# Optimization experiments

Hardware: AMD Instinct MI355X
Metric: run time of the kernel (lower is better)

The kernel has to match this reference:

```python
import jax, jax.numpy as jnp
import numpy as np

NUM_HEADS = 8
TOPK_RATIO = 0.1


def setup_inputs() -> dict:
    key = jax.random.key(0)
    ks = jax.random.split(key, 5)
    B, N, C = 1, 8192, 512
    S = 16              # num_frames
    K = 4               # clusters
    x = jax.random.normal(ks[0], (B, N, C), dtype=jnp.float32)
    w_qkv = jax.random.normal(ks[1], (3 * C, C), dtype=jnp.float32) * (C ** -0.5)
    b_qkv = jax.random.normal(ks[2], (3 * C,), dtype=jnp.float32) * 0.02
    w_proj = jax.random.normal(ks[3], (C, C), dtype=jnp.float32) * (C ** -0.5)
    b_proj = jax.random.normal(ks[4], (C,), dtype=jnp.float32) * 0.02
    keyframes = jnp.arange(K, dtype=jnp.int64 if jax.config.jax_enable_x64 else jnp.int32) * (S // K)  # [0,4,8,12]
    clusters = jnp.arange(S, dtype=keyframes.dtype).reshape(K, S // K)  # 4 clusters of 4 frames
    return {"x": x, "w_qkv": w_qkv, "b_qkv": b_qkv, "w_proj": w_proj,
            "b_proj": b_proj, "keyframes": keyframes, "clusters": clusters,
            "num_frames": S}


def _hierarchy_attn(q, k, v, keyframes, clusters, num_frames):
    # q,k,v: [B,H,N,D]
    B, H, N, D = q.shape
    scale = D ** -0.5
    tpf = N // num_frames                     # tokens per frame
    K = clusters.shape[0]
    tok = jnp.arange(tpf)
    # keyframe query token indices: [K*tpf]
    key_q_idx = (keyframes[:, None] * tpf + tok[None, :]).reshape(-1)
    q_proto = q[:, :, key_q_idx, :]           # [B,H,K*tpf,D]
    # proto attention scores vs all keys: [B,H,K*tpf,N]
    scores = jnp.einsum('bhqd,bhnd->bhqn', q_proto * scale, k)
    # aggregate per cluster (over batch, heads, keyframe tokens) -> [K,N]
    agg = scores.reshape(B, H, K, tpf, N).mean(axis=(0, 1, 3))
    topk_num = max(1, int(tpf * K * TOPK_RATIO))
    _, topk_idx = jax.lax.top_k(agg, topk_num)          # [K, T]
    # cluster query token indices: [K, M] with M = frames_per_cluster*tpf
    cluster_q_idx = (clusters[:, :, None] * tpf + tok[None, None, :]).reshape(K, -1)
    q_c = q[:, :, cluster_q_idx, :]           # [B,H,K,M,D]
    k_c = k[:, :, topk_idx, :]                # [B,H,K,T,D]
    v_c = v[:, :, topk_idx, :]                # [B,H,K,T,D]
    attn = jax.nn.softmax(jnp.einsum('bhkmd,bhktd->bhkmt', q_c * scale, k_c), axis=-1)
    x_c = jnp.einsum('bhkmt,bhktd->bhkmd', attn, v_c)   # [B,H,K,M,D]
    x_out = jnp.zeros_like(q)
    x_out = x_out.at[:, :, cluster_q_idx.reshape(-1), :].set(
        x_c.reshape(B, H, K * x_c.shape[3], D))
    return x_out


def reference(x, w_qkv, b_qkv, w_proj, b_proj, keyframes, clusters, num_frames):
    B, N, C = x.shape
    H = NUM_HEADS
    D = C // H
    qkv = (x @ w_qkv.T + b_qkv).reshape(B, N, 3, H, D)
    qkv = jnp.transpose(qkv, (2, 0, 3, 1, 4))           # [3,B,H,N,D]
    q, k, v = qkv[0], qkv[1], qkv[2]
    x_out = _hierarchy_attn(q, k, v, keyframes, clusters, num_frames)  # [B,H,N,D]
    x_out = jnp.transpose(x_out, (0, 2, 1, 3)).reshape(B, N, C)
    return x_out @ w_proj.T + b_proj
```

## Files before the change

### kernel.cpp

```cpp
#include <hip/hip_runtime.h>
#include <hip/hip_bf16.h>

#define N_TOK 8192
#define C_DIM 512
#define NH 8
#define DH 64
#define KCLUST 4
#define TPF 512
#define TOPK 204
#define KVPAD 256
#define MPC 2048

#define WS_WQH    0
#define WS_WPH    393216
#define WS_QHI    524288
#define WS_KC     2621440
#define WS_VC     2883584
#define WS_XAHI   3145728
#define WS_XBARP  5242880
#define WS_QBAR   5275648
#define WS_G      5277696
#define WS_AGG    5279744
#define WS_TOPK   5312512

using frag16 = __attribute__((ext_vector_type(8))) short;
using f32x4  = __attribute__((ext_vector_type(4))) float;

__device__ __forceinline__ unsigned short f2bf(float x) {
  unsigned u = __float_as_uint(x);
  return (unsigned short)((u + 0x7fffu + ((u >> 16) & 1u)) >> 16);
}
__device__ __forceinline__ float bf2f(unsigned short h) {
  return __uint_as_float(((unsigned)h) << 16);
}
__device__ __forceinline__ unsigned pkbf(float a, float b) {
  __hip_bfloat162 t = __float22bfloat162_rn(make_float2(a, b));
  return *reinterpret_cast<unsigned*>(&t);
}

__global__ __launch_bounds__(256) void prep(
    const float* __restrict__ w_qkv, const float* __restrict__ w_proj,
    const float* __restrict__ x, const int* __restrict__ keyframes,
    unsigned short* __restrict__ wqh, unsigned short* __restrict__ wph,
    float* __restrict__ xbarp) {
  const int bx = blockIdx.x, tid = threadIdx.x;
  if (bx < 1024) {
    const float* src = (bx < 768) ? w_qkv : w_proj;
    unsigned short* dst = (bx < 768) ? wqh : wph;
    int i = ((bx < 768) ? bx : (bx - 768)) * 256 + tid;
    float4 v = reinterpret_cast<const float4*>(src)[i];
    reinterpret_cast<uint2*>(dst)[i] = make_uint2(pkbf(v.x, v.y), pkbf(v.z, v.w));
  } else {
    int b = bx - 1024, kk = b >> 4, s = b & 15;
    int base = keyframes[kk] * TPF + s * 32;
    float a0 = 0.f, a1 = 0.f;
    for (int t = 0; t < 32; t++) {
      a0 += x[(size_t)(base + t) * C_DIM + tid];
      a1 += x[(size_t)(base + t) * C_DIM + tid + 256];
    }
    xbarp[(kk * 16 + s) * C_DIM + tid] = a0;
    xbarp[(kk * 16 + s) * C_DIM + tid + 256] = a1;
  }
}

#define APAN 1032
#define BUFS 8256
__global__ __launch_bounds__(256) void gemm_qkv2(
    const float* __restrict__ x, const unsigned short* __restrict__ Bhi,
    const float* __restrict__ bias, const int* __restrict__ topk,
    unsigned short* __restrict__ qhi, unsigned short* __restrict__ kc,
    unsigned short* __restrict__ vc) {
  __shared__ short pool[17408];
  const int tid = threadIdx.x;
  const int bid = blockIdx.x;
  const bool is_kv = bid >= 256;
  int j0, m0 = 0, kk = 0, mloc = 0;
  if (!is_kv) {
    const int grp = bid >> 5;
    const int rem = bid & 31;
    j0 = (rem >> 3) * 128;
    m0 = (grp * 8 + (rem & 7)) * 128;
  } else {
    const int b2 = bid - 256;
    kk = b2 >> 4;
    const int sub = b2 & 15;
    mloc = (sub >> 3) * 128;
    j0 = 512 + (sub & 7) * 128;
  }
  const int wave = tid >> 6, lane = tid & 63;
  const int wr = wave >> 1, wc = wave & 1;
  const int qd = lane >> 4, ln = lane & 15;

  const int r0 = tid >> 2, p0 = tid & 3;
  const int r1 = r0 + 64;
  const float4 *pA0, *pA1;
  if (!is_kv) {
    pA0 = reinterpret_cast<const float4*>(x + (size_t)(m0 + r0) * C_DIM) + p0 * 2;
    pA1 = reinterpret_cast<const float4*>(x + (size_t)(m0 + r1) * C_DIM) + p0 * 2;
  } else {
    int t0i = mloc + r0, t1i = mloc + r1;
    if (t0i > TOPK - 1) t0i = TOPK - 1;
    if (t1i > TOPK - 1) t1i = TOPK - 1;
    const int tok0 = topk[kk * TOPK + t0i];
    const int tok1 = topk[kk * TOPK + t1i];
    pA0 = reinterpret_cast<const float4*>(x + (size_t)tok0 * C_DIM) + p0 * 2;
    pA1 = reinterpret_cast<const float4*>(x + (size_t)tok1 * C_DIM) + p0 * 2;
  }
  const unsigned short* pB0 = Bhi + (size_t)(j0 + r0) * C_DIM + p0 * 8;
  const unsigned short* pB1 = Bhi + (size_t)(j0 + r1) * C_DIM + p0 * 8;

  f32x4 acc[4][4] = {};

  float4 fa[4];
  uint4 rb[2];
  fa[0] = pA0[0]; fa[1] = pA0[1];
  fa[2] = pA1[0]; fa[3] = pA1[1];
  rb[0] = *reinterpret_cast<const uint4*>(pB0);
  rb[1] = *reinterpret_cast<const uint4*>(pB1);

  {
    *reinterpret_cast<uint4*>(&pool[p0 * APAN + r0 * 8]) =
        make_uint4(pkbf(fa[0].x, fa[0].y), pkbf(fa[0].z, fa[0].w),
                   pkbf(fa[1].x, fa[1].y), pkbf(fa[1].z, fa[1].w));
    *reinterpret_cast<uint4*>(&pool[p0 * APAN + r1 * 8]) =
        make_uint4(pkbf(fa[2].x, fa[2].y), pkbf(fa[2].z, fa[2].w),
                   pkbf(fa[3].x, fa[3].y), pkbf(fa[3].z, fa[3].w));
    *reinterpret_cast<uint4*>(&pool[4 * APAN + p0 * APAN + r0 * 8]) = rb[0];
    *reinterpret_cast<uint4*>(&pool[4 * APAN + p0 * APAN + r1 * 8]) = rb[1];
  }
  __syncthreads();

  int cur = 0;
#pragma unroll
  for (int it = 0; it < 16; it++) {
    if (it < 15) {
      int k4 = (it + 1) * 8;
      fa[0] = pA0[k4]; fa[1] = pA0[k4 + 1];
      fa[2] = pA1[k4]; fa[3] = pA1[k4 + 1];
      rb[0] = *reinterpret_cast<const uint4*>(pB0 + (it + 1) * 32);
      rb[1] = *reinterpret_cast<const uint4*>(pB1 + (it + 1) * 32);
    }
    const int bb = cur * BUFS;
    frag16 a_h[4], b_h[4];
#pragma unroll
    for (int i = 0; i < 4; i++) {
      int row = wr * 64 + i * 16 + ln;
      a_h[i] = *reinterpret_cast<const frag16*>(&pool[bb + qd * APAN + row * 8]);
    }
#pragma unroll
    for (int j = 0; j < 4; j++) {
      int row = wc * 64 + j * 16 + ln;
      b_h[j] = *reinterpret_cast<const frag16*>(&pool[bb + 4 * APAN + qd * APAN + row * 8]);
    }
#pragma unroll
    for (int i = 0; i < 4; i++)
#pragma unroll
      for (int j = 0; j < 4; j++)
        acc[i][j] = __builtin_amdgcn_mfma_f32_16x16x32_bf16(a_h[i], b_h[j], acc[i][j], 0, 0, 0);

    if (it < 15) {
      const int nb = (cur ^ 1) * BUFS;
      *reinterpret_cast<uint4*>(&pool[nb + p0 * APAN + r0 * 8]) =
          make_uint4(pkbf(fa[0].x, fa[0].y), pkbf(fa[0].z, fa[0].w),
                     pkbf(fa[1].x, fa[1].y), pkbf(fa[1].z, fa[1].w));
      *reinterpret_cast<uint4*>(&pool[nb + p0 * APAN + r1 * 8]) =
          make_uint4(pkbf(fa[2].x, fa[2].y), pkbf(fa[2].z, fa[2].w),
                     pkbf(fa[3].x, fa[3].y), pkbf(fa[3].z, fa[3].w));
      *reinterpret_cast<uint4*>(&pool[nb + 4 * APAN + p0 * APAN + r0 * 8]) = rb[0];
      *reinterpret_cast<uint4*>(&pool[nb + 4 * APAN + p0 * APAN + r1 * 8]) = rb[1];
    }
    __syncthreads();
    cur ^= 1;
  }

  const int sel = j0 >> 9;
  const float qscale = (sel == 0) ? 0.125f : 1.0f;
  short* sh = pool;

#pragma unroll
  for (int i = 0; i < 4; i++)
#pragma unroll
    for (int j = 0; j < 4; j++) {
      int jcol = wc * 64 + j * 16 + ln;
      float bv = bias[j0 + jcol];
#pragma unroll
      for (int r = 0; r < 4; r++) {
        int mrow = wr * 64 + i * 16 + qd * 4 + r;
        sh[mrow * 136 + jcol] = (short)f2bf((acc[i][j][r] + bv) * qscale);
      }
    }
  __syncthreads();
  if (!is_kv) {
#pragma unroll
    for (int p = 0; p < 8; p++) {
      int u = tid + p * 256;
      int row = u >> 4, c = (u & 15) * 8;
      int hh = ((j0 + c) >> 6) & 7, d0 = c & 63;
      *reinterpret_cast<uint4*>(qhi + ((size_t)hh * N_TOK + m0 + row) * DH + d0) =
          *reinterpret_cast<const uint4*>(&sh[row * 136 + c]);
    }
  } else {
    unsigned short* dstc = (sel == 1) ? kc : vc;
#pragma unroll
    for (int p = 0; p < 8; p++) {
      int u = tid + p * 256;
      int row = u >> 4, c = (u & 15) * 8;
      int hh = ((j0 + c) >> 6) & 7, d0 = c & 63;
      *reinterpret_cast<uint4*>(
          dstc + (((size_t)kk * 8 + hh) * KVPAD + mloc + row) * DH + d0) =
          *reinterpret_cast<const uint4*>(&sh[row * 136 + c]);
    }
  }
}

__global__ __launch_bounds__(256) void qbar_k(const float* __restrict__ w_qkv,
                                              const float* __restrict__ b_qkv,
                                              const float* __restrict__ xbarp,
                                              float* __restrict__ qbar) {
  __shared__ float xs[C_DIM];
  __shared__ float red[256];
  int blk = blockIdx.x, h = blk >> 2, kk = blk & 3, tid = threadIdx.x;
  for (int i = tid; i < C_DIM; i += 256) {
    float a = 0.f;
    for (int s = 0; s < 16; s++) a += xbarp[(kk * 16 + s) * C_DIM + i];
    xs[i] = a * (1.f / 512.f);
  }
  __syncthreads();
  int d = tid & 63, pp = tid >> 6;
  const float* wrow = w_qkv + (size_t)(h * 64 + d) * C_DIM + pp * 128;
  float a = 0.f;
  for (int c = 0; c < 128; c++) a += wrow[c] * xs[pp * 128 + c];
  red[tid] = a;
  __syncthreads();
  if (pp == 0)
    qbar[(h * 4 + kk) * 64 + d] = red[d] + red[64 + d] + red[128 + d] + red[192 + d] +
                                  b_qkv[h * 64 + d];
}

__global__ __launch_bounds__(256) void g_full(const float* __restrict__ w_qkv,
                                              const float* __restrict__ qbar,
                                              float* __restrict__ g) {
  __shared__ float qs[C_DIM];
  __shared__ float red[256];
  int kk = blockIdx.x >> 3, cs = blockIdx.x & 7, tid = threadIdx.x;
  for (int i = tid; i < C_DIM; i += 256)
    qs[i] = qbar[((i >> 6) * 4 + kk) * 64 + (i & 63)];
  __syncthreads();
  int jg = tid >> 6, c = tid & 63;
  float a = 0.f;
  const float* wk = w_qkv + (size_t)C_DIM * C_DIM + cs * 64 + c;
  for (int j = jg * 128; j < jg * 128 + 128; j++)
    a += qs[j] * wk[(size_t)j * C_DIM];
  red[tid] = a;
  __syncthreads();
  if (jg == 0)
    g[kk * C_DIM + cs * 64 + c] = red[c] + red[64 + c] + red[128 + c] + red[192 + c];
}

__global__ __launch_bounds__(256) void agg2_kernel(const float* __restrict__ x,
                                                   const float* __restrict__ g,
                                                   float* __restrict__ agg) {
  __shared__ float gs[KCLUST][C_DIM];
  int tid = threadIdx.x;
  for (int i = tid; i < KCLUST * C_DIM; i += 256) gs[i >> 9][i & 511] = g[i];
  __syncthreads();
  int wave = tid >> 6, lane = tid & 63;
  int n = blockIdx.x * 4 + wave;
  const float4* xp = reinterpret_cast<const float4*>(x + (size_t)n * C_DIM);
  float4 xa = xp[lane], xb = xp[lane + 64];
  float a[4];
#pragma unroll
  for (int kk = 0; kk < 4; kk++) {
    const float4* gpv = reinterpret_cast<const float4*>(&gs[kk][0]);
    float4 ga = gpv[lane], gb2 = gpv[lane + 64];
    a[kk] = xa.x * ga.x + xa.y * ga.y + xa.z * ga.z + xa.w * ga.w +
            xb.x * gb2.x + xb.y * gb2.y + xb.z * gb2.z + xb.w * gb2.w;
  }
#pragma unroll
  for (int off = 32; off >= 1; off >>= 1) {
    a[0] += __shfl_xor(a[0], off);
    a[1] += __shfl_xor(a[1], off);
    a[2] += __shfl_xor(a[2], off);
    a[3] += __shfl_xor(a[3], off);
  }
  if (lane == 0) {
    agg[0 * N_TOK + n] = a[0];
    agg[1 * N_TOK + n] = a[1];
    agg[2 * N_TOK + n] = a[2];
    agg[3 * N_TOK + n] = a[3];
  }
}

__device__ __forceinline__ int block_scan_incl(int v, int* wsum, int tid) {
  int lane = tid & 63, wv = tid >> 6;
#pragma unroll
  for (int off = 1; off < 64; off <<= 1) {
    int t = __shfl_up(v, off, 64);
    if (lane >= off) v += t;
  }
  if (lane == 63) wsum[wv] = v;
  __syncthreads();
  if (wv > 0) v += wsum[0];
  if (wv > 1) v += wsum[1];
  if (wv > 2) v += wsum[2];
  __syncthreads();
  return v;
}

__global__ __launch_bounds__(256) void topk_kernel(const float* __restrict__ agg,
                                                   int* __restrict__ topk) {
  __shared__ unsigned sk[N_TOK];
  __shared__ int hist[256];
  __shared__ int scn[256];
  __shared__ int wsum[4];
  __shared__ int sel_bin, sel_rem;
  int kk = blockIdx.x, tid = threadIdx.x;
  const float* row = agg + (size_t)kk * N_TOK;

  for (int i = tid; i < N_TOK; i += 256) {
    unsigned u = __float_as_uint(row[i]);
    sk[i] = (u & 0x80000000u) ? ~u : (u | 0x80000000u);
  }
  __syncthreads();

  unsigned prefix = 0;
  int remaining = TOPK;
#pragma unroll
  for (int rnd = 3; rnd >= 0; rnd--) {
    int shift = rnd * 8;
    hist[tid] = 0;
    __syncthreads();
    for (int i = tid; i < N_TOK; i += 256) {
      unsigned key = sk[i];
      bool in = (rnd == 3) || ((key >> (shift + 8)) == prefix);
      if (in) atomicAdd(&hist[(key >> shift) & 255], 1);
    }
    __syncthreads();
    int sv = block_scan_incl(hist[255 - tid], wsum, tid);
    scn[tid] = sv;
    __syncthreads();
    int b = tid;
    int cgt = (b == 255) ? 0 : scn[254 - b];
    if (cgt < remaining && remaining <= cgt + hist[b]) {
      sel_bin = b;
      sel_rem = remaining - cgt;
    }
    __syncthreads();
    prefix = (prefix << 8) | (unsigned)sel_bin;
    remaining = sel_rem;
    __syncthreads();
  }
  unsigned kth = prefix;

  int* out_row = topk + kk * TOPK;
  int base = tid * 32;

  int cA = 0;
  for (int i = 0; i < 32; i++) cA += (sk[base + i] > kth) ? 1 : 0;
  int sA = block_scan_incl(cA, wsum, tid);
  scn[tid] = sA;
  __syncthreads();
  int exclA = sA - cA;
  int G = scn[255];
  int p = exclA;
  for (int i = 0; i < 32; i++)
    if (sk[base + i] > kth) out_row[p++] = base + i;
  __syncthreads();

  int cB = 0;
  for (int i = 0; i < 32; i++) cB += (sk[base + i] == kth) ? 1 : 0;
  int sB = block_scan_incl(cB, wsum, tid);
  int exclB = sB - cB;
  int pos = G + exclB;
  for (int i = 0; i < 32; i++) {
    if (sk[base + i] == kth) {
      if (pos < TOPK) out_row[pos] = base + i;
      pos++;
    }
  }
}

__global__ __launch_bounds__(256) void flash_mfma(
    const unsigned short* __restrict__ qhi, const unsigned short* __restrict__ kc,
    const unsigned short* __restrict__ vc, const int* __restrict__ clusters,
    unsigned short* __restrict__ xahi) {
  __shared__ short Ks[64 * 72];
  __shared__ short Vs[64 * 72];
  __shared__ short Ps[128 * 72];
  const int tid = threadIdx.x;
  const int qb = blockIdx.x, kk = blockIdx.y, h = blockIdx.z;
  const int wave = tid >> 6, lane = tid & 63;
  const int ln = lane & 15, qd = lane >> 4;

  const int q_local0 = qb * 128;
  const int frame = clusters[kk * 4 + (q_local0 >> 9)];
  const int tokbase = frame * TPF + (q_local0 & 511);
  const size_t kvbase = ((size_t)kk * 8 + h) * KVPAD * DH;

  frag16 qa_h[2][2];
#pragma unroll
  for (int mt = 0; mt < 2; mt++) {
    const int tok_m = tokbase + wave * 32 + mt * 16 + ln;
    const unsigned short* qr_h = qhi + ((size_t)h * N_TOK + tok_m) * DH;
#pragma unroll
    for (int s = 0; s < 2; s++)
      qa_h[mt][s] = *reinterpret_cast<const frag16*>(qr_h + s * 32 + qd * 8);
  }

  f32x4 acc_o[2][4] = {};
  float lsum[2][4] = {};

  for (int t0 = 0; t0 < 192; t0 += 64) {
#pragma unroll
    for (int i = 0; i < 2; i++) {
      int u = tid + i * 256;
      int r = u >> 3, oct = u & 7;
      *reinterpret_cast<frag16*>(&Ks[r * 72 + oct * 8]) =
          *reinterpret_cast<const frag16*>(kc + kvbase + (size_t)(t0 + r) * DH + oct * 8);
    }
    {
      int tk = (tid & 15) * 4, td = (tid >> 4) * 4;
      uint2 w2[4];
#pragma unroll
      for (int i = 0; i < 4; i++)
        w2[i] = *reinterpret_cast<const uint2*>(vc + kvbase + (size_t)(t0 + tk + i) * DH + td);
#pragma unroll
      for (int dd = 0; dd < 4; dd++) {
        unsigned s0 = (dd < 2) ? (w2[0].x >> (16 * dd)) : (w2[0].y >> (16 * (dd - 2)));
        unsigned s1 = (dd < 2) ? (w2[1].x >> (16 * dd)) : (w2[1].y >> (16 * (dd - 2)));
        unsigned s2 = (dd < 2) ? (w2[2].x >> (16 * dd)) : (w2[2].y >> (16 * (dd - 2)));
        unsigned s3 = (dd < 2) ? (w2[3].x >> (16 * dd)) : (w2[3].y >> (16 * (dd - 2)));
        *reinterpret_cast<uint2*>(&Vs[(td + dd) * 72 + tk]) =
            make_uint2((s0 & 0xffffu) | (s1 << 16), (s2 & 0xffffu) | (s3 << 16));
      }
    }
    __syncthreads();

#pragma unroll
    for (int mt = 0; mt < 2; mt++) {
      f32x4 sacc[4] = {};
#pragma unroll
      for (int c = 0; c < 4; c++) {
#pragma unroll
        for (int s = 0; s < 2; s++) {
          frag16 bh = *reinterpret_cast<const frag16*>(&Ks[(c * 16 + ln) * 72 + s * 32 + qd * 8]);
          sacc[c] = __builtin_amdgcn_mfma_f32_16x16x32_bf16(qa_h[mt][s], bh, sacc[c], 0, 0, 0);
        }
      }
#pragma unroll
      for (int c = 0; c < 4; c++) {
#pragma unroll
        for (int r = 0; r < 4; r++) {
          float p = __expf(sacc[c][r]);
          lsum[mt][r] += p;
          Ps[(wave * 32 + mt * 16 + qd * 4 + r) * 72 + c * 16 + ln] = (short)f2bf(p);
        }
      }
    }

#pragma unroll
    for (int mt = 0; mt < 2; mt++)
#pragma unroll
      for (int s = 0; s < 2; s++) {
        frag16 pa = *reinterpret_cast<const frag16*>(
            &Ps[(wave * 32 + mt * 16 + ln) * 72 + s * 32 + qd * 8]);
#pragma unroll
        for (int dt = 0; dt < 4; dt++) {
          frag16 vb = *reinterpret_cast<const frag16*>(&Vs[(dt * 16 + ln) * 72 + s * 32 + qd * 8]);
          acc_o[mt][dt] = __builtin_amdgcn_mfma_f32_16x16x32_bf16(pa, vb, acc_o[mt][dt], 0, 0, 0);
        }
      }
    __syncthreads();
  }

  {
    const int t0 = 192;
#pragma unroll
    for (int i = 0; i < 2; i++) {
      int u = tid + i * 256;
      int r = u >> 3, oct = u & 7;
      *reinterpret_cast<frag16*>(&Ks[r * 72 + oct * 8]) =
          *reinterpret_cast<const frag16*>(kc + kvbase + (size_t)(t0 + r) * DH + oct * 8);
    }
    {
      int tk = (tid & 15) * 4, td = (tid >> 4) * 4;
      uint2 w2[4];
#pragma unroll
      for (int i = 0; i < 4; i++)
        w2[i] = *reinterpret_cast<const uint2*>(vc + kvbase + (size_t)(t0 + tk + i) * DH + td);
#pragma unroll
      for (int dd = 0; dd < 4; dd++) {
        unsigned s0 = (dd < 2) ? (w2[0].x >> (16 * dd)) : (w2[0].y >> (16 * (dd - 2)));
        unsigned s1 = (dd < 2) ? (w2[1].x >> (16 * dd)) : (w2[1].y >> (16 * (dd - 2)));
        unsigned s2 = (dd < 2) ? (w2[2].x >> (16 * dd)) : (w2[2].y >> (16 * (dd - 2)));
        unsigned s3 = (dd < 2) ? (w2[3].x >> (16 * dd)) : (w2[3].y >> (16 * (dd - 2)));
        *reinterpret_cast<uint2*>(&Vs[(td + dd) * 72 + tk]) =
            make_uint2((s0 & 0xffffu) | (s1 << 16), (s2 & 0xffffu) | (s3 << 16));
      }
    }
    __syncthreads();

#pragma unroll
    for (int mt = 0; mt < 2; mt++) {
      f32x4 sacc = {};
#pragma unroll
      for (int s = 0; s < 2; s++) {
        frag16 bh = *reinterpret_cast<const frag16*>(&Ks[ln * 72 + s * 32 + qd * 8]);
        sacc = __builtin_amdgcn_mfma_f32_16x16x32_bf16(qa_h[mt][s], bh, sacc, 0, 0, 0);
      }
#pragma unroll
      for (int r = 0; r < 4; r++) {
        float p = (ln < 12) ? __expf(sacc[r]) : 0.f;
        lsum[mt][r] += p;
        int prow = (wave * 32 + mt * 16 + qd * 4 + r) * 72;
        Ps[prow + ln] = (short)f2bf(p);
        Ps[prow + 16 + ln] = 0;
      }
    }

#pragma unroll
    for (int mt = 0; mt < 2; mt++) {
      frag16 pa = *reinterpret_cast<const frag16*>(
          &Ps[(wave * 32 + mt * 16 + ln) * 72 + qd * 8]);
#pragma unroll
      for (int dt = 0; dt < 4; dt++) {
        frag16 vb = *reinterpret_cast<const frag16*>(&Vs[(dt * 16 + ln) * 72 + qd * 8]);
        acc_o[mt][dt] = __builtin_amdgcn_mfma_f32_16x16x32_bf16(pa, vb, acc_o[mt][dt], 0, 0, 0);
      }
    }
  }

#pragma unroll
  for (int mt = 0; mt < 2; mt++)
#pragma unroll
    for (int r = 0; r < 4; r++) {
      float l = lsum[mt][r];
      l += __shfl_xor(l, 1);
      l += __shfl_xor(l, 2);
      l += __shfl_xor(l, 4);
      l += __shfl_xor(l, 8);
      lsum[mt][r] = 1.f / l;
    }

#pragma unroll
  for (int mt = 0; mt < 2; mt++)
#pragma unroll
    for (int dt = 0; dt < 4; dt++)
#pragma unroll
      for (int r = 0; r < 4; r++)
        Ps[(wave * 32 + mt * 16 + qd * 4 + r) * 72 + dt * 16 + ln] =
            (short)f2bf(acc_o[mt][dt][r] * lsum[mt][r]);
  __syncthreads();
#pragma unroll
  for (int p = 0; p < 4; p++) {
    int u = tid + p * 256;
    int row = u >> 3, c = (u & 7) * 8;
    *reinterpret_cast<uint4*>(xahi + (size_t)(tokbase + row) * C_DIM + h * DH + c) =
        *reinterpret_cast<const uint4*>(&Ps[row * 72 + c]);
  }
}

__global__ __launch_bounds__(256) void gemm_proj(
    const unsigned short* __restrict__ Ahi, const unsigned short* __restrict__ Bhi,
    const float* __restrict__ bias, float* __restrict__ out) {
  __shared__ short pool[12288];
  short* As = pool;
  short* Bs = pool + 4096;
  const int tid = threadIdx.x;
  const int bid = blockIdx.x;
  const int grp = bid / 32;
  const int rem = bid - grp * 32;
  const int jblk = rem >> 3;
  const int m_idx = grp * 8 + (rem & 7);
  const int j0 = jblk * 128;
  const int m0 = m_idx * 64;
  const int wave = tid >> 6, lane = tid & 63;
  const int rh = wave >> 1, ch = wave & 1;
  const int qd = lane >> 4, ln = lane & 15;

  const int arow = tid & 63, ap = tid >> 6;
  const int brow = tid & 127, bp = tid >> 7;
  const unsigned short* pA = Ahi + (size_t)(m0 + arow) * C_DIM + ap * 8;
  const unsigned short* pB0 = Bhi + (size_t)(j0 + brow) * C_DIM + bp * 8;
  const unsigned short* pB1 = pB0 + 16;

  f32x4 acc[2][4] = {};

  uint4 ra = *reinterpret_cast<const uint4*>(pA);
  uint4 rb0 = *reinterpret_cast<const uint4*>(pB0);
  uint4 rb1 = *reinterpret_cast<const uint4*>(pB1);
  *reinterpret_cast<uint4*>(&As[ap * 512 + arow * 8]) = ra;
  *reinterpret_cast<uint4*>(&Bs[bp * 1024 + brow * 8]) = rb0;
  *reinterpret_cast<uint4*>(&Bs[(bp + 2) * 1024 + brow * 8]) = rb1;
  __syncthreads();

  int cur = 0;
#pragma unroll
  for (int it = 0; it < 16; it++) {
    if (it < 15) {
      int k = (it + 1) * 32;
      ra = *reinterpret_cast<const uint4*>(pA + k);
      rb0 = *reinterpret_cast<const uint4*>(pB0 + k);
      rb1 = *reinterpret_cast<const uint4*>(pB1 + k);
    }
    frag16 a_h[2], b_h[4];
#pragma unroll
    for (int i = 0; i < 2; i++)
      a_h[i] = *reinterpret_cast<const frag16*>(&As[cur * 2048 + qd * 512 + (rh * 32 + i * 16 + ln) * 8]);
#pragma unroll
    for (int j = 0; j < 4; j++)
      b_h[j] = *reinterpret_cast<const frag16*>(&Bs[cur * 4096 + qd * 1024 + (ch * 64 + j * 16 + ln) * 8]);
#pragma unroll
    for (int i = 0; i < 2; i++)
#pragma unroll
      for (int j = 0; j < 4; j++)
        acc[i][j] = __builtin_amdgcn_mfma_f32_16x16x32_bf16(a_h[i], b_h[j], acc[i][j], 0, 0, 0);
    if (it < 15) {
      int nxt = cur ^ 1;
      *reinterpret_cast<uint4*>(&As[nxt * 2048 + ap * 512 + arow * 8]) = ra;
      *reinterpret_cast<uint4*>(&Bs[nxt * 4096 + bp * 1024 + brow * 8]) = rb0;
      *reinterpret_cast<uint4*>(&Bs[nxt * 4096 + (bp + 2) * 1024 + brow * 8]) = rb1;
      __syncthreads();
      cur = nxt;
    }
  }

  float* sh32 = reinterpret_cast<float*>(pool);
#pragma unroll
  for (int chp = 0; chp < 2; chp++) {
    __syncthreads();
    if (ch == chp) {
#pragma unroll
      for (int i = 0; i < 2; i++)
#pragma unroll
        for (int j = 0; j < 4; j++) {
          int jcol = j * 16 + ln;
          float bv = bias[j0 + chp * 64 + jcol];
#pragma unroll
          for (int r = 0; r < 4; r++)
            sh32[(rh * 32 + i * 16 + qd * 4 + r) * 68 + jcol] = acc[i][j][r] + bv;
        }
    }
    __syncthreads();
#pragma unroll
    for (int p = 0; p < 4; p++) {
      int u = tid + p * 256;
      int row = u >> 4, c4 = (u & 15) * 4;
      *reinterpret_cast<float4*>(out + (size_t)(m0 + row) * C_DIM + j0 + chp * 64 + c4) =
          *reinterpret_cast<const float4*>(&sh32[row * 68 + c4]);
    }
  }
}

extern "C" void kernel_launch(void* const* d_in, const int* in_sizes, int n_in,
                              void* d_out, int out_size, void* d_ws, size_t ws_size,
                              hipStream_t stream) {
  const float* x = (const float*)d_in[0];
  const float* w_qkv = (const float*)d_in[1];
  const float* b_qkv = (const float*)d_in[2];
  const float* w_proj = (const float*)d_in[3];
  const float* b_proj = (const float*)d_in[4];
  const int* keyframes = (const int*)d_in[5];
  const int* clusters = (const int*)d_in[6];
  float* out = (float*)d_out;
  float* ws = (float*)d_ws;

  unsigned short* wqh = (unsigned short*)(ws + WS_WQH);
  unsigned short* wph = (unsigned short*)(ws + WS_WPH);
  unsigned short* qhi = (unsigned short*)(ws + WS_QHI);
  unsigned short* kc = (unsigned short*)(ws + WS_KC);
  unsigned short* vc = (unsigned short*)(ws + WS_VC);
  unsigned short* xahi = (unsigned short*)(ws + WS_XAHI);
  float* xbarp = ws + WS_XBARP;
  float* qbar = ws + WS_QBAR;
  float* g = ws + WS_G;
  float* agg = ws + WS_AGG;
  int* topkp = (int*)(ws + WS_TOPK);

  prep<<<1088, 256, 0, stream>>>(w_qkv, w_proj, x, keyframes, wqh, wph, xbarp);
  qbar_k<<<32, 256, 0, stream>>>(w_qkv, b_qkv, xbarp, qbar);
  g_full<<<32, 256, 0, stream>>>(w_qkv, qbar, g);
  agg2_kernel<<<2048, 256, 0, stream>>>(x, g, agg);
  topk_kernel<<<4, 256, 0, stream>>>(agg, topkp);
  gemm_qkv2<<<320, 256, 0, stream>>>(x, wqh, b_qkv, topkp, qhi, kc, vc);
  flash_mfma<<<dim3(MPC / 128, KCLUST, NH), 256, 0, stream>>>(
      qhi, kc, vc, clusters, xahi);
  gemm_proj<<<512, 256, 0, stream>>>(xahi, wph, b_proj, out);
}
```

Before: 204.8 us.

## Fuse ranking kernels into one persistent kernel with grid barriers

Merges qbar, g, aggregation and top-k kernels into a single 256-block kernel separated by atomic-counter grid barriers, with the barrier counters reset in the prep kernel. This removes three kernel launches and the gaps between them on a chain of tiny kernels. The cost is spin-waiting barriers that rely on all 256 blocks being co-resident, and the aggregation now runs on 256 blocks in a loop instead of 2048 blocks.

New measurement: 239.9 us. 17.2% more time.

```diff
diff --git a/kernel.cpp b/kernel.cpp
--- a/kernel.cpp
+++ b/kernel.cpp
@@ -22,6 +22,7 @@
 #define WS_G      5277696
 #define WS_AGG    5279744
 #define WS_TOPK   5312512
+#define WS_BAR    5313536
 
 using frag16 = __attribute__((ext_vector_type(8))) short;
 using f32x4  = __attribute__((ext_vector_type(4))) float;
@@ -42,8 +43,9 @@
     const float* __restrict__ w_qkv, const float* __restrict__ w_proj,
     const float* __restrict__ x, const int* __restrict__ keyframes,
     unsigned short* __restrict__ wqh, unsigned short* __restrict__ wph,
-    float* __restrict__ xbarp) {
+    float* __restrict__ xbarp, int* __restrict__ bar) {
   const int bx = blockIdx.x, tid = threadIdx.x;
+  if (bx == 1024 && tid < 8) bar[tid] = 0;
   if (bx < 1024) {
     const float* src = (bx < 768) ? w_qkv : w_proj;
     unsigned short* dst = (bx < 768) ? wqh : wph;
@@ -213,84 +215,6 @@
   }
 }
 
-__global__ __launch_bounds__(256) void qbar_k(const float* __restrict__ w_qkv,
-                                              const float* __restrict__ b_qkv,
-                                              const float* __restrict__ xbarp,
-                                              float* __restrict__ qbar) {
-  __shared__ float xs[C_DIM];
-  __shared__ float red[256];
-  int blk = blockIdx.x, h = blk >> 2, kk = blk & 3, tid = threadIdx.x;
-  for (int i = tid; i < C_DIM; i += 256) {
-    float a = 0.f;
-    for (int s = 0; s < 16; s++) a += xbarp[(kk * 16 + s) * C_DIM + i];
-    xs[i] = a * (1.f / 512.f);
-  }
-  __syncthreads();
-  int d = tid & 63, pp = tid >> 6;
-  const float* wrow = w_qkv + (size_t)(h * 64 + d) * C_DIM + pp * 128;
-  float a = 0.f;
-  for (int c = 0; c < 128; c++) a += wrow[c] * xs[pp * 128 + c];
-  red[tid] = a;
-  __syncthreads();
-  if (pp == 0)
-    qbar[(h * 4 + kk) * 64 + d] = red[d] + red[64 + d] + red[128 + d] + red[192 + d] +
-                                  b_qkv[h * 64 + d];
-}
-
-__global__ __launch_bounds__(256) void g_full(const float* __restrict__ w_qkv,
-                                              const float* __restrict__ qbar,
-                                              float* __restrict__ g) {
-  __shared__ float qs[C_DIM];
-  __shared__ float red[256];
-  int kk = blockIdx.x >> 3, cs = blockIdx.x & 7, tid = threadIdx.x;
-  for (int i = tid; i < C_DIM; i += 256)
-    qs[i] = qbar[((i >> 6) * 4 + kk) * 64 + (i & 63)];
-  __syncthreads();
-  int jg = tid >> 6, c = tid & 63;
-  float a = 0.f;
-  const float* wk = w_qkv + (size_t)C_DIM * C_DIM + cs * 64 + c;
-  for (int j = jg * 128; j < jg * 128 + 128; j++)
-    a += qs[j] * wk[(size_t)j * C_DIM];
-  red[tid] = a;
-  __syncthreads();
-  if (jg == 0)
-    g[kk * C_DIM + cs * 64 + c] = red[c] + red[64 + c] + red[128 + c] + red[192 + c];
-}
-
-__global__ __launch_bounds__(256) void agg2_kernel(const float* __restrict__ x,
-                                                   const float* __restrict__ g,
-                                                   float* __restrict__ agg) {
-  __shared__ float gs[KCLUST][C_DIM];
-  int tid = threadIdx.x;
-  for (int i = tid; i < KCLUST * C_DIM; i += 256) gs[i >> 9][i & 511] = g[i];
-  __syncthreads();
-  int wave = tid >> 6, lane = tid & 63;
-  int n = blockIdx.x * 4 + wave;
-  const float4* xp = reinterpret_cast<const float4*>(x + (size_t)n * C_DIM);
-  float4 xa = xp[lane], xb = xp[lane + 64];
-  float a[4];
-#pragma unroll
-  for (int kk = 0; kk < 4; kk++) {
-    const float4* gpv = reinterpret_cast<const float4*>(&gs[kk][0]);
-    float4 ga = gpv[lane], gb2 = gpv[lane + 64];
-    a[kk] = xa.x * ga.x + xa.y * ga.y + xa.z * ga.z + xa.w * ga.w +
-            xb.x * gb2.x + xb.y * gb2.y + xb.z * gb2.z + xb.w * gb2.w;
-  }
-#pragma unroll
-  for (int off = 32; off >= 1; off >>= 1) {
-    a[0] += __shfl_xor(a[0], off);
-    a[1] += __shfl_xor(a[1], off);
-    a[2] += __shfl_xor(a[2], off);
-    a[3] += __shfl_xor(a[3], off);
-  }
-  if (lane == 0) {
-    agg[0 * N_TOK + n] = a[0];
-    agg[1 * N_TOK + n] = a[1];
-    agg[2 * N_TOK + n] = a[2];
-    agg[3 * N_TOK + n] = a[3];
-  }
-}
-
 __device__ __forceinline__ int block_scan_incl(int v, int* wsum, int tid) {
   int lane = tid & 63, wv = tid >> 6;
 #pragma unroll
@@ -307,75 +231,170 @@
   return v;
 }
 
-__global__ __launch_bounds__(256) void topk_kernel(const float* __restrict__ agg,
-                                                   int* __restrict__ topk) {
-  __shared__ unsigned sk[N_TOK];
-  __shared__ int hist[256];
-  __shared__ int scn[256];
-  __shared__ int wsum[4];
-  __shared__ int sel_bin, sel_rem;
-  int kk = blockIdx.x, tid = threadIdx.x;
-  const float* row = agg + (size_t)kk * N_TOK;
-
-  for (int i = tid; i < N_TOK; i += 256) {
-    unsigned u = __float_as_uint(row[i]);
-    sk[i] = (u & 0x80000000u) ? ~u : (u | 0x80000000u);
-  }
+__device__ __forceinline__ void gbar(int* __restrict__ bar, int idx, int nblk,
+                                     int tid) {
   __syncthreads();
-
-  unsigned prefix = 0;
-  int remaining = TOPK;
-#pragma unroll
-  for (int rnd = 3; rnd >= 0; rnd--) {
-    int shift = rnd * 8;
-    hist[tid] = 0;
-    __syncthreads();
+  if (tid == 0) {
+    __threadfence();
+    atomicAdd(&bar[idx], 1);
+    while (atomicAdd(&bar[idx], 0) < nblk) __builtin_amdgcn_s_sleep(8);
+    __threadfence();
+  }
+  __syncthreads();
+}
+
+__global__ __launch_bounds__(256) void rank_fused(
+    const float* __restrict__ w_qkv, const float* __restrict__ b_qkv,
+    const float* __restrict__ xbarp, float* __restrict__ qbar,
+    float* __restrict__ g, const float* __restrict__ x,
+    float* __restrict__ agg, int* __restrict__ topk, int* __restrict__ bar) {
+  __shared__ __align__(16) char smem[34848];
+  const int bid = blockIdx.x, tid = threadIdx.x;
+
+  if (bid < 32) {
+    float* xs = reinterpret_cast<float*>(smem);
+    float* red = xs + C_DIM;
+    int h = bid >> 2, kk = bid & 3;
+    for (int i = tid; i < C_DIM; i += 256) {
+      float a = 0.f;
+      for (int s = 0; s < 16; s++) a += xbarp[(kk * 16 + s) * C_DIM + i];
+      xs[i] = a * (1.f / 512.f);
+    }
+    __syncthreads();
+    int d = tid & 63, pp = tid >> 6;
+    const float* wrow = w_qkv + (size_t)(h * 64 + d) * C_DIM + pp * 128;
+    float a = 0.f;
+    for (int c = 0; c < 128; c++) a += wrow[c] * xs[pp * 128 + c];
+    red[tid] = a;
+    __syncthreads();
+    if (pp == 0)
+      qbar[(h * 4 + kk) * 64 + d] = red[d] + red[64 + d] + red[128 + d] + red[192 + d] +
+                                    b_qkv[h * 64 + d];
+  }
+  gbar(bar, 0, 256, tid);
+
+  if (bid < 32) {
+    float* qs = reinterpret_cast<float*>(smem);
+    float* red = qs + C_DIM;
+    int kk = bid >> 3, cs = bid & 7;
+    for (int i = tid; i < C_DIM; i += 256)
+      qs[i] = qbar[((i >> 6) * 4 + kk) * 64 + (i & 63)];
+    __syncthreads();
+    int jg = tid >> 6, c = tid & 63;
+    float a = 0.f;
+    const float* wk = w_qkv + (size_t)C_DIM * C_DIM + cs * 64 + c;
+    for (int j = jg * 128; j < jg * 128 + 128; j++)
+      a += qs[j] * wk[(size_t)j * C_DIM];
+    red[tid] = a;
+    __syncthreads();
+    if (jg == 0)
+      g[kk * C_DIM + cs * 64 + c] = red[c] + red[64 + c] + red[128 + c] + red[192 + c];
+  }
+  gbar(bar, 1, 256, tid);
+
+  {
+    float* gs = reinterpret_cast<float*>(smem);
+    for (int i = tid; i < KCLUST * C_DIM; i += 256) gs[i] = g[i];
+    __syncthreads();
+    int wave = tid >> 6, lane = tid & 63;
+    for (int vb = bid; vb < 2048; vb += 256) {
+      int n = vb * 4 + wave;
+      const float4* xp = reinterpret_cast<const float4*>(x + (size_t)n * C_DIM);
+      float4 xa = xp[lane], xb = xp[lane + 64];
+      float a[4];
+#pragma unroll
+      for (int kk = 0; kk < 4; kk++) {
+        const float4* gpv = reinterpret_cast<const float4*>(gs + kk * C_DIM);
+        float4 ga = gpv[lane], gb2 = gpv[lane + 64];
+        a[kk] = xa.x * ga.x + xa.y * ga.y + xa.z * ga.z + xa.w * ga.w +
+                xb.x * gb2.x + xb.y * gb2.y + xb.z * gb2.z + xb.w * gb2.w;
+      }
+#pragma unroll
+      for (int off = 32; off >= 1; off >>= 1) {
+        a[0] += __shfl_xor(a[0], off);
+        a[1] += __shfl_xor(a[1], off);
+        a[2] += __shfl_xor(a[2], off);
+        a[3] += __shfl_xor(a[3], off);
+      }
+      if (lane == 0) {
+        agg[0 * N_TOK + n] = a[0];
+        agg[1 * N_TOK + n] = a[1];
+        agg[2 * N_TOK + n] = a[2];
+        agg[3 * N_TOK + n] = a[3];
+      }
+    }
+  }
+  gbar(bar, 2, 256, tid);
+
+  if (bid < 4) {
+    unsigned* sk = reinterpret_cast<unsigned*>(smem);
+    int* hist = reinterpret_cast<int*>(smem + 32768);
+    int* scn = reinterpret_cast<int*>(smem + 33792);
+    int* wsum = reinterpret_cast<int*>(smem + 34816);
+    int* selv = reinterpret_cast<int*>(smem + 34832);
+    int kk = bid;
+    const float* row = agg + (size_t)kk * N_TOK;
+
     for (int i = tid; i < N_TOK; i += 256) {
-      unsigned key = sk[i];
-      bool in = (rnd == 3) || ((key >> (shift + 8)) == prefix);
-      if (in) atomicAdd(&hist[(key >> shift) & 255], 1);
-    }
-    __syncthreads();
-    int sv = block_scan_incl(hist[255 - tid], wsum, tid);
-    scn[tid] = sv;
-    __syncthreads();
-    int b = tid;
-    int cgt = (b == 255) ? 0 : scn[254 - b];
-    if (cgt < remaining && remaining <= cgt + hist[b]) {
-      sel_bin = b;
-      sel_rem = remaining - cgt;
-    }
-    __syncthreads();
-    prefix = (prefix << 8) | (unsigned)sel_bin;
-    remaining = sel_rem;
-    __syncthreads();
-  }
-  unsigned kth = prefix;
-
-  int* out_row = topk + kk * TOPK;
-  int base = tid * 32;
-
-  int cA = 0;
-  for (int i = 0; i < 32; i++) cA += (sk[base + i] > kth) ? 1 : 0;
-  int sA = block_scan_incl(cA, wsum, tid);
-  scn[tid] = sA;
-  __syncthreads();
-  int exclA = sA - cA;
-  int G = scn[255];
-  int p = exclA;
-  for (int i = 0; i < 32; i++)
-    if (sk[base + i] > kth) out_row[p++] = base + i;
-  __syncthreads();
-
-  int cB = 0;
-  for (int i = 0; i < 32; i++) cB += (sk[base + i] == kth) ? 1 : 0;
-  int sB = block_scan_incl(cB, wsum, tid);
-  int exclB = sB - cB;
-  int pos = G + exclB;
-  for (int i = 0; i < 32; i++) {
-    if (sk[base + i] == kth) {
-      if (pos < TOPK) out_row[pos] = base + i;
-      pos++;
+      unsigned u = __float_as_uint(row[i]);
+      sk[i] = (u & 0x80000000u) ? ~u : (u | 0x80000000u);
+    }
+    __syncthreads();
+
+    unsigned prefix = 0;
+    int remaining = TOPK;
+#pragma unroll
+    for (int rnd = 3; rnd >= 0; rnd--) {
+      int shift = rnd * 8;
+      hist[tid] = 0;
+      __syncthreads();
+      for (int i = tid; i < N_TOK; i += 256) {
+        unsigned key = sk[i];
+        bool in = (rnd == 3) || ((key >> (shift + 8)) == prefix);
+        if (in) atomicAdd(&hist[(key >> shift) & 255], 1);
+      }
+      __syncthreads();
+      int sv = block_scan_incl(hist[255 - tid], wsum, tid);
+      scn[tid] = sv;
+      __syncthreads();
+      int b = tid;
+      int cgt = (b == 255) ? 0 : scn[254 - b];
+      if (cgt < remaining && remaining <= cgt + hist[b]) {
+        selv[0] = b;
+        selv[1] = remaining - cgt;
+      }
+      __syncthreads();
+      prefix = (prefix << 8) | (unsigned)selv[0];
+      remaining = selv[1];
+      __syncthreads();
+    }
+    unsigned kth = prefix;
+
+    int* out_row = topk + kk * TOPK;
+    int base = tid * 32;
+
+    int cA = 0;
+    for (int i = 0; i < 32; i++) cA += (sk[base + i] > kth) ? 1 : 0;
+    int sA = block_scan_incl(cA, wsum, tid);
+    scn[tid] = sA;
+    __syncthreads();
+    int exclA = sA - cA;
+    int G = scn[255];
+    int p = exclA;
+    for (int i = 0; i < 32; i++)
+      if (sk[base + i] > kth) out_row[p++] = base + i;
+    __syncthreads();
+
+    int cB = 0;
+    for (int i = 0; i < 32; i++) cB += (sk[base + i] == kth) ? 1 : 0;
+    int sB = block_scan_incl(cB, wsum, tid);
+    int exclB = sB - cB;
+    int pos = G + exclB;
+    for (int i = 0; i < 32; i++) {
+      if (sk[base + i] == kth) {
+        if (pos < TOPK) out_row[pos] = base + i;
+        pos++;
+      }
     }
   }
 }
@@ -676,12 +695,11 @@
   float* g = ws + WS_G;
   float* agg = ws + WS_AGG;
   int* topkp = (int*)(ws + WS_TOPK);
-
-  prep<<<1088, 256, 0, stream>>>(w_qkv, w_proj, x, keyframes, wqh, wph, xbarp);
-  qbar_k<<<32, 256, 0, stream>>>(w_qkv, b_qkv, xbarp, qbar);
-  g_full<<<32, 256, 0, stream>>>(w_qkv, qbar, g);
-  agg2_kernel<<<2048, 256, 0, stream>>>(x, g, agg);
-  topk_kernel<<<4, 256, 0, stream>>>(agg, topkp);
+  int* bar = (int*)(ws + WS_BAR);
+
+  prep<<<1088, 256, 0, stream>>>(w_qkv, w_proj, x, keyframes, wqh, wph, xbarp, bar);
+  rank_fused<<<256, 256, 0, stream>>>(w_qkv, b_qkv, xbarp, qbar, g, x, agg,
+                                      topkp, bar);
   gemm_qkv2<<<320, 256, 0, stream>>>(x, wqh, b_qkv, topkp, qhi, kc, vc);
   flash_mfma<<<dim3(MPC / 128, KCLUST, NH), 256, 0, stream>>>(
       qhi, kc, vc, clusters, xahi);
```

## Fuse qbar and g kernels, move weight conversion into agg kernel

Applied to the files above, without the earlier changes.

Merges the qbar and g projection kernels into one kernel, where each block recomputes the full per-cluster query mean over all heads before projecting through the key weights. It also moves the bf16 weight conversion out of the prep kernel and into the agg kernel as extra blocks, so prep only computes the keyframe sums. The aim is to save one launch and to overlap weight conversion with the aggregation pass instead of running it on the critical path ahead of qbar. In exchange, each of the 32 fused blocks repeats the 8-head query matvec (8x redundant reads of the query weights) and runs serially over heads with syncs.

Result: slower. 234.9 us (+14.7%).

```diff
diff --git a/kernel.cpp b/kernel.cpp
--- a/kernel.cpp
+++ b/kernel.cpp
@@ -38,28 +38,191 @@
   return *reinterpret_cast<unsigned*>(&t);
 }
 
-__global__ __launch_bounds__(256) void prep(
-    const float* __restrict__ w_qkv, const float* __restrict__ w_proj,
+__global__ __launch_bounds__(256) void prep_xbar(
     const float* __restrict__ x, const int* __restrict__ keyframes,
-    unsigned short* __restrict__ wqh, unsigned short* __restrict__ wph,
     float* __restrict__ xbarp) {
-  const int bx = blockIdx.x, tid = threadIdx.x;
-  if (bx < 1024) {
+  const int b = blockIdx.x, tid = threadIdx.x;
+  int kk = b >> 4, s = b & 15;
+  int base = keyframes[kk] * TPF + s * 32;
+  float a0 = 0.f, a1 = 0.f;
+  for (int t = 0; t < 32; t++) {
+    a0 += x[(size_t)(base + t) * C_DIM + tid];
+    a1 += x[(size_t)(base + t) * C_DIM + tid + 256];
+  }
+  xbarp[(kk * 16 + s) * C_DIM + tid] = a0;
+  xbarp[(kk * 16 + s) * C_DIM + tid + 256] = a1;
+}
+
+__global__ __launch_bounds__(256) void qg_fused(
+    const float* __restrict__ w_qkv, const float* __restrict__ b_qkv,
+    const float* __restrict__ xbarp, float* __restrict__ g) {
+  __shared__ float xs[C_DIM];
+  __shared__ float red[256];
+  __shared__ float qloc[C_DIM];
+  const int kk = blockIdx.x >> 3, cs = blockIdx.x & 7, tid = threadIdx.x;
+
+  for (int i = tid; i < C_DIM; i += 256) {
+    float a = 0.f;
+    for (int s = 0; s < 16; s++) a += xbarp[(kk * 16 + s) * C_DIM + i];
+    xs[i] = a * (1.f / 512.f);
+  }
+  __syncthreads();
+
+  const int d = tid & 63, pp = tid >> 6;
+  for (int h = 0; h < 8; h++) {
+    const float* wrow = w_qkv + (size_t)(h * 64 + d) * C_DIM + pp * 128;
+    float a = 0.f;
+    for (int c = 0; c < 128; c++) a += wrow[c] * xs[pp * 128 + c];
+    red[tid] = a;
+    __syncthreads();
+    if (pp == 0)
+      qloc[h * 64 + d] = red[d] + red[64 + d] + red[128 + d] + red[192 + d] +
+                         b_qkv[h * 64 + d];
+    __syncthreads();
+  }
+
+  const int jg = tid >> 6, c = tid & 63;
+  float a = 0.f;
+  const float* wk = w_qkv + (size_t)C_DIM * C_DIM + cs * 64 + c;
+  for (int j = jg * 128; j < jg * 128 + 128; j++)
+    a += qloc[j] * wk[(size_t)j * C_DIM];
+  red[tid] = a;
+  __syncthreads();
+  if (jg == 0)
+    g[kk * C_DIM + cs * 64 + c] = red[c] + red[64 + c] + red[128 + c] + red[192 + c];
+}
+
+__global__ __launch_bounds__(256) void agg_wcvt(
+    const float* __restrict__ x, const float* __restrict__ g,
+    float* __restrict__ agg, const float* __restrict__ w_qkv,
+    const float* __restrict__ w_proj, unsigned short* __restrict__ wqh,
+    unsigned short* __restrict__ wph) {
+  __shared__ float gs[KCLUST][C_DIM];
+  const int bid = blockIdx.x, tid = threadIdx.x;
+  if (bid >= 2048) {
+    int bx = bid - 2048;
     const float* src = (bx < 768) ? w_qkv : w_proj;
     unsigned short* dst = (bx < 768) ? wqh : wph;
     int i = ((bx < 768) ? bx : (bx - 768)) * 256 + tid;
     float4 v = reinterpret_cast<const float4*>(src)[i];
     reinterpret_cast<uint2*>(dst)[i] = make_uint2(pkbf(v.x, v.y), pkbf(v.z, v.w));
-  } else {
-    int b = bx - 1024, kk = b >> 4, s = b & 15;
-    int base = keyframes[kk] * TPF + s * 32;
-    float a0 = 0.f, a1 = 0.f;
-    for (int t = 0; t < 32; t++) {
-      a0 += x[(size_t)(base + t) * C_DIM + tid];
-      a1 += x[(size_t)(base + t) * C_DIM + tid + 256];
-    }
-    xbarp[(kk * 16 + s) * C_DIM + tid] = a0;
-    xbarp[(kk * 16 + s) * C_DIM + tid + 256] = a1;
+    return;
+  }
+  for (int i = tid; i < KCLUST * C_DIM; i += 256) gs[i >> 9][i & 511] = g[i];
+  __syncthreads();
+  int wave = tid >> 6, lane = tid & 63;
+  int n = bid * 4 + wave;
+  const float4* xp = reinterpret_cast<const float4*>(x + (size_t)n * C_DIM);
+  float4 xa = xp[lane], xb = xp[lane + 64];
+  float a[4];
+#pragma unroll
+  for (int kk = 0; kk < 4; kk++) {
+    const float4* gpv = reinterpret_cast<const float4*>(&gs[kk][0]);
+    float4 ga = gpv[lane], gb2 = gpv[lane + 64];
+    a[kk] = xa.x * ga.x + xa.y * ga.y + xa.z * ga.z + xa.w * ga.w +
+            xb.x * gb2.x + xb.y * gb2.y + xb.z * gb2.z + xb.w * gb2.w;
+  }
+#pragma unroll
+  for (int off = 32; off >= 1; off >>= 1) {
+    a[0] += __shfl_xor(a[0], off);
+    a[1] += __shfl_xor(a[1], off);
+    a[2] += __shfl_xor(a[2], off);
+    a[3] += __shfl_xor(a[3], off);
+  }
+  if (lane == 0) {
+    agg[0 * N_TOK + n] = a[0];
+    agg[1 * N_TOK + n] = a[1];
+    agg[2 * N_TOK + n] = a[2];
+    agg[3 * N_TOK + n] = a[3];
+  }
+}
+
+__device__ __forceinline__ int block_scan_incl(int v, int* wsum, int tid) {
+  int lane = tid & 63, wv = tid >> 6;
+#pragma unroll
+  for (int off = 1; off < 64; off <<= 1) {
+    int t = __shfl_up(v, off, 64);
+    if (lane >= off) v += t;
+  }
+  if (lane == 63) wsum[wv] = v;
+  __syncthreads();
+  if (wv > 0) v += wsum[0];
+  if (wv > 1) v += wsum[1];
+  if (wv > 2) v += wsum[2];
+  __syncthreads();
+  return v;
+}
+
+__global__ __launch_bounds__(256) void topk_kernel(const float* __restrict__ agg,
+                                                   int* __restrict__ topk) {
+  __shared__ unsigned sk[N_TOK];
+  __shared__ int hist[256];
+  __shared__ int scn[256];
+  __shared__ int wsum[4];
+  __shared__ int sel_bin, sel_rem;
+  int kk = blockIdx.x, tid = threadIdx.x;
+  const float* row = agg + (size_t)kk * N_TOK;
+
+  for (int i = tid; i < N_TOK; i += 256) {
+    unsigned u = __float_as_uint(row[i]);
+    sk[i] = (u & 0x80000000u) ? ~u : (u | 0x80000000u);
+  }
+  __syncthreads();
+
+  unsigned prefix = 0;
+  int remaining = TOPK;
+#pragma unroll
+  for (int rnd = 3; rnd >= 0; rnd--) {
+    int shift = rnd * 8;
+    hist[tid] = 0;
+    __syncthreads();
+    for (int i = tid; i < N_TOK; i += 256) {
+      unsigned key = sk[i];
+      bool in = (rnd == 3) || ((key >> (shift + 8)) == prefix);
+      if (in) atomicAdd(&hist[(key >> shift) & 255], 1);
+    }
+    __syncthreads();
+    int sv = block_scan_incl(hist[255 - tid], wsum, tid);
+    scn[tid] = sv;
+    __syncthreads();
+    int b = tid;
+    int cgt = (b == 255) ? 0 : scn[254 - b];
+    if (cgt < remaining && remaining <= cgt + hist[b]) {
+      sel_bin = b;
+      sel_rem = remaining - cgt;
+    }
+    __syncthreads();
+    prefix = (prefix << 8) | (unsigned)sel_bin;
+    remaining = sel_rem;
+    __syncthreads();
+  }
+  unsigned kth = prefix;
+
+  int* out_row = topk + kk * TOPK;
+  int base = tid * 32;
+
+  int cA = 0;
+  for (int i = 0; i < 32; i++) cA += (sk[base + i] > kth) ? 1 : 0;
+  int sA = block_scan_incl(cA, wsum, tid);
+  scn[tid] = sA;
+  __syncthreads();
+  int exclA = sA - cA;
+  int G = scn[255];
+  int p = exclA;
+  for (int i = 0; i < 32; i++)
+    if (sk[base + i] > kth) out_row[p++] = base + i;
+  __syncthreads();
+
+  int cB = 0;
+  for (int i = 0; i < 32; i++) cB += (sk[base + i] == kth) ? 1 : 0;
+  int sB = block_scan_incl(cB, wsum, tid);
+  int exclB = sB - cB;
+  int pos = G + exclB;
+  for (int i = 0; i < 32; i++) {
+    if (sk[base + i] == kth) {
+      if (pos < TOPK) out_row[pos] = base + i;
+      pos++;
+    }
   }
 }
 
@@ -213,173 +376,6 @@
   }
 }
 
-__global__ __launch_bounds__(256) void qbar_k(const float* __restrict__ w_qkv,
-                                              const float* __restrict__ b_qkv,
-                                              const float* __restrict__ xbarp,
-                                              float* __restrict__ qbar) {
-  __shared__ float xs[C_DIM];
-  __shared__ float red[256];
-  int blk = blockIdx.x, h = blk >> 2, kk = blk & 3, tid = threadIdx.x;
-  for (int i = tid; i < C_DIM; i += 256) {
-    float a = 0.f;
-    for (int s = 0; s < 16; s++) a += xbarp[(kk * 16 + s) * C_DIM + i];
-    xs[i] = a * (1.f / 512.f);
-  }
-  __syncthreads();
-  int d = tid & 63, pp = tid >> 6;
-  const float* wrow = w_qkv + (size_t)(h * 64 + d) * C_DIM + pp * 128;
-  float a = 0.f;
-  for (int c = 0; c < 128; c++) a += wrow[c] * xs[pp * 128 + c];
-  red[tid] = a;
-  __syncthreads();
-  if (pp == 0)
-    qbar[(h * 4 + kk) * 64 + d] = red[d] + red[64 + d] + red[128 + d] + red[192 + d] +
-                                  b_qkv[h * 64 + d];
-}
-
-__global__ __launch_bounds__(256) void g_full(const float* __restrict__ w_qkv,
-                                              const float* __restrict__ qbar,
-                                              float* __restrict__ g) {
-  __shared__ float qs[C_DIM];
-  __shared__ float red[256];
-  int kk = blockIdx.x >> 3, cs = blockIdx.x & 7, tid = threadIdx.x;
-  for (int i = tid; i < C_DIM; i += 256)
-    qs[i] = qbar[((i >> 6) * 4 + kk) * 64 + (i & 63)];
-  __syncthreads();
-  int jg = tid >> 6, c = tid & 63;
-  float a = 0.f;
-  const float* wk = w_qkv + (size_t)C_DIM * C_DIM + cs * 64 + c;
-  for (int j = jg * 128; j < jg * 128 + 128; j++)
-    a += qs[j] * wk[(size_t)j * C_DIM];
-  red[tid] = a;
-  __syncthreads();
-  if (jg == 0)
-    g[kk * C_DIM + cs * 64 + c] = red[c] + red[64 + c] + red[128 + c] + red[192 + c];
-}
-
-__global__ __launch_bounds__(256) void agg2_kernel(const float* __restrict__ x,
-                                                   const float* __restrict__ g,
-                                                   float* __restrict__ agg) {
-  __shared__ float gs[KCLUST][C_DIM];
-  int tid = threadIdx.x;
-  for (int i = tid; i < KCLUST * C_DIM; i += 256) gs[i >> 9][i & 511] = g[i];
-  __syncthreads();
-  int wave = tid >> 6, lane = tid & 63;
-  int n = blockIdx.x * 4 + wave;
-  const float4* xp = reinterpret_cast<const float4*>(x + (size_t)n * C_DIM);
-  float4 xa = xp[lane], xb = xp[lane + 64];
-  float a[4];
-#pragma unroll
-  for (int kk = 0; kk < 4; kk++) {
-    const float4* gpv = reinterpret_cast<const float4*>(&gs[kk][0]);
-    float4 ga = gpv[lane], gb2 = gpv[lane + 64];
-    a[kk] = xa.x * ga.x + xa.y * ga.y + xa.z * ga.z + xa.w * ga.w +
-            xb.x * gb2.x + xb.y * gb2.y + xb.z * gb2.z + xb.w * gb2.w;
-  }
-#pragma unroll
-  for (int off = 32; off >= 1; off >>= 1) {
-    a[0] += __shfl_xor(a[0], off);
-    a[1] += __shfl_xor(a[1], off);
-    a[2] += __shfl_xor(a[2], off);
-    a[3] += __shfl_xor(a[3], off);
-  }
-  if (lane == 0) {
-    agg[0 * N_TOK + n] = a[0];
-    agg[1 * N_TOK + n] = a[1];
-    agg[2 * N_TOK + n] = a[2];
-    agg[3 * N_TOK + n] = a[3];
-  }
-}
-
-__device__ __forceinline__ int block_scan_incl(int v, int* wsum, int tid) {
-  int lane = tid & 63, wv = tid >> 6;
-#pragma unroll
-  for (int off = 1; off < 64; off <<= 1) {
-    int t = __shfl_up(v, off, 64);
-    if (lane >= off) v += t;
-  }
-  if (lane == 63) wsum[wv] = v;
-  __syncthreads();
-  if (wv > 0) v += wsum[0];
-  if (wv > 1) v += wsum[1];
-  if (wv > 2) v += wsum[2];
-  __syncthreads();
-  return v;
-}
-
-__global__ __launch_bounds__(256) void topk_kernel(const float* __restrict__ agg,
-                                                   int* __restrict__ topk) {
-  __shared__ unsigned sk[N_TOK];
-  __shared__ int hist[256];
-  __shared__ int scn[256];
-  __shared__ int wsum[4];
-  __shared__ int sel_bin, sel_rem;
-  int kk = blockIdx.x, tid = threadIdx.x;
-  const float* row = agg + (size_t)kk * N_TOK;
-
-  for (int i = tid; i < N_TOK; i += 256) {
-    unsigned u = __float_as_uint(row[i]);
-    sk[i] = (u & 0x80000000u) ? ~u : (u | 0x80000000u);
-  }
-  __syncthreads();
-
-  unsigned prefix = 0;
-  int remaining = TOPK;
-#pragma unroll
-  for (int rnd = 3; rnd >= 0; rnd--) {
-    int shift = rnd * 8;
-    hist[tid] = 0;
-    __syncthreads();
-    for (int i = tid; i < N_TOK; i += 256) {
-      unsigned key = sk[i];
-      bool in = (rnd == 3) || ((key >> (shift + 8)) == prefix);
-      if (in) atomicAdd(&hist[(key >> shift) & 255], 1);
-    }
-    __syncthreads();
-    int sv = block_scan_incl(hist[255 - tid], wsum, tid);
-    scn[tid] = sv;
-    __syncthreads();
-    int b = tid;
-    int cgt = (b == 255) ? 0 : scn[254 - b];
-    if (cgt < remaining && remaining <= cgt + hist[b]) {
-      sel_bin = b;
-      sel_rem = remaining - cgt;
-    }
-    __syncthreads();
-    prefix = (prefix << 8) | (unsigned)sel_bin;
-    remaining = sel_rem;
-    __syncthreads();
-  }
-  unsigned kth = prefix;
-
-  int* out_row = topk + kk * TOPK;
-  int base = tid * 32;
-
-  int cA = 0;
-  for (int i = 0; i < 32; i++) cA += (sk[base + i] > kth) ? 1 : 0;
-  int sA = block_scan_incl(cA, wsum, tid);
-  scn[tid] = sA;
-  __syncthreads();
-  int exclA = sA - cA;
-  int G = scn[255];
-  int p = exclA;
-  for (int i = 0; i < 32; i++)
-    if (sk[base + i] > kth) out_row[p++] = base + i;
-  __syncthreads();
-
-  int cB = 0;
-  for (int i = 0; i < 32; i++) cB += (sk[base + i] == kth) ? 1 : 0;
-  int sB = block_scan_incl(cB, wsum, tid);
-  int exclB = sB - cB;
-  int pos = G + exclB;
-  for (int i = 0; i < 32; i++) {
-    if (sk[base + i] == kth) {
-      if (pos < TOPK) out_row[pos] = base + i;
-      pos++;
-    }
-  }
-}
-
 __global__ __launch_bounds__(256) void flash_mfma(
     const unsigned short* __restrict__ qhi, const unsigned short* __restrict__ kc,
     const unsigned short* __restrict__ vc, const int* __restrict__ clusters,
@@ -672,15 +668,13 @@
   unsigned short* vc = (unsigned short*)(ws + WS_VC);
   unsigned short* xahi = (unsigned short*)(ws + WS_XAHI);
   float* xbarp = ws + WS_XBARP;
-  float* qbar = ws + WS_QBAR;
   float* g = ws + WS_G;
   float* agg = ws + WS_AGG;
   int* topkp = (int*)(ws + WS_TOPK);
 
-  prep<<<1088, 256, 0, stream>>>(w_qkv, w_proj, x, keyframes, wqh, wph, xbarp);
-  qbar_k<<<32, 256, 0, stream>>>(w_qkv, b_qkv, xbarp, qbar);
-  g_full<<<32, 256, 0, stream>>>(w_qkv, qbar, g);
-  agg2_kernel<<<2048, 256, 0, stream>>>(x, g, agg);
+  prep_xbar<<<64, 256, 0, stream>>>(x, keyframes, xbarp);
+  qg_fused<<<32, 256, 0, stream>>>(w_qkv, b_qkv, xbarp, g);
+  agg_wcvt<<<3072, 256, 0, stream>>>(x, g, agg, w_qkv, w_proj, wqh, wph);
   topk_kernel<<<4, 256, 0, stream>>>(agg, topkp);
   gemm_qkv2<<<320, 256, 0, stream>>>(x, wqh, b_qkv, topkp, qhi, kc, vc);
   flash_mfma<<<dim3(MPC / 128, KCLUST, NH), 256, 0, stream>>>(
```
